# Kernel optimization log

Hardware: AMD Instinct MI355X
Metric: run time of the kernel (lower is better)

## Reference

```python
import jax, jax.numpy as jnp
import numpy as np

N = 500000   # total nodes in batched graph
B = 8192     # number of graphs
H = 128      # hidden_dim
L = 3        # num_layer -> feature_dim F = H*L = 384
F = H * L
S2S_STEPS = 3
VOCAB = 143


def setup_inputs() -> dict:
    key = jax.random.key(0)
    ks = jax.random.split(key, 12)
    sc = 0.02
    unit_type = jax.random.randint(ks[0], (N,), 0, VOCAB)
    # sorted segment ids covering every graph (contiguous, all B segments non-empty)
    node2graph = (jnp.arange(N) * B) // N
    return {
        'unit_type': unit_type,
        'node2graph': node2graph,
        'embed':    jax.random.normal(ks[1], (VOCAB, H)) * sc,
        'msg_W1':   jax.random.normal(ks[2], (H, 2 * H)) * sc,
        'msg_b1':   jnp.zeros((H,)),
        'msg_W2':   jax.random.normal(ks[3], (H, H)) * sc,
        'msg_b2':   jnp.zeros((H,)),
        'gru_Wih':  jax.random.normal(ks[4], (3 * H, H)) * sc,
        'gru_Whh':  jax.random.normal(ks[5], (3 * H, H)) * sc,
        'gru_bih':  jnp.zeros((3 * H,)),
        'gru_bhh':  jnp.zeros((3 * H,)),
        'lstm_Wih': jax.random.normal(ks[6], (4 * F, 2 * F)) * sc,
        'lstm_Whh': jax.random.normal(ks[7], (4 * F, F)) * sc,
        'lstm_bih': jnp.zeros((4 * F,)),
        'lstm_bhh': jnp.zeros((4 * F,)),
    }


def _gru_step(x, h, Wih, Whh, bih, bhh):
    # single-timestep PyTorch GRU cell; gate order r, z, n
    gi = x @ Wih.T + bih
    gh = h @ Whh.T + bhh
    ir, iz, inn = jnp.split(gi, 3, axis=-1)
    hr, hz, hn = jnp.split(gh, 3, axis=-1)
    r = jax.nn.sigmoid(ir + hr)
    z = jax.nn.sigmoid(iz + hz)
    n = jnp.tanh(inn + r * hn)
    return (1.0 - z) * n + z * h


def _lstm_step(x, h, c, Wih, Whh, bih, bhh):
    # single-timestep PyTorch LSTM cell; gate order i, f, g, o
    g = x @ Wih.T + bih + h @ Whh.T + bhh
    i, f, gc, o = jnp.split(g, 4, axis=-1)
    c = jax.nn.sigmoid(f) * c + jax.nn.sigmoid(i) * jnp.tanh(gc)
    h = jax.nn.sigmoid(o) * jnp.tanh(c)
    return h, c


def reference(unit_type, node2graph, embed, msg_W1, msg_b1, msg_W2, msg_b2,
              gru_Wih, gru_Whh, gru_bih, gru_bhh,
              lstm_Wih, lstm_Whh, lstm_bih, lstm_bhh):
    # --- node update stack ---
    layer_input = embed[unit_type]          # [N, H]
    hx = layer_input                        # GRU hidden state (1 layer)
    hiddens = []
    for _ in range(L):
        x2 = jnp.concatenate([layer_input, layer_input], axis=-1)   # [N, 2H]
        msg = jnp.maximum(x2 @ msg_W1.T + msg_b1, 0.0) @ msg_W2.T + msg_b2
        hx = _gru_step(msg, hx, gru_Wih, gru_Whh, gru_bih, gru_bhh)
        hiddens.append(hx)
        layer_input = hx
    node_feature = jnp.concatenate(hiddens, axis=-1)                # [N, F]

    # --- Set2Set readout ---
    h = jnp.zeros((B, F), dtype=node_feature.dtype)
    c = jnp.zeros((B, F), dtype=node_feature.dtype)
    q_star = jnp.zeros((B, 2 * F), dtype=node_feature.dtype)
    for _ in range(S2S_STEPS):
        h, c = _lstm_step(q_star, h, c, lstm_Wih, lstm_Whh, lstm_bih, lstm_bhh)
        q = h                                                       # [B, F]
        logits = jnp.sum(q[node2graph] * node_feature, axis=-1)     # [N]
        m = jax.ops.segment_max(logits, node2graph, num_segments=B,
                                indices_are_sorted=True)
        e = jnp.exp(logits - m[node2graph])
        z = jax.ops.segment_sum(e, node2graph, num_segments=B,
                                indices_are_sorted=True)
        att = e / z[node2graph]                                     # [N]
        pooled = jax.ops.segment_sum(att[:, None] * node_feature, node2graph,
                                     num_segments=B, indices_are_sorted=True)
        q_star = jnp.concatenate([q, pooled], axis=-1)              # [B, 2F]

    return q_star, node_feature
```

## Files before the change

kernel.cpp:

```cpp
#include <hip/hip_runtime.h>

typedef unsigned short u16;
typedef unsigned int   u32;
typedef u16 bfx8 __attribute__((ext_vector_type(8)));
typedef __bf16 bf16x8 __attribute__((ext_vector_type(8)));
typedef float  f32x4  __attribute__((ext_vector_type(4)));

#define NH  128
#define NF  384
#define K2F 768
#define NG4 1536

__device__ __forceinline__ float bf2f(u16 u){ return __uint_as_float(((u32)u) << 16); }
__device__ __forceinline__ u16 f2bf(float f){
  __bf16 h = (__bf16)f;
  return __builtin_bit_cast(u16, h);
}
__device__ __forceinline__ float fsig(float x){ return 1.0f / (1.0f + __expf(-x)); }
__device__ __forceinline__ float ftanh(float x){ return 1.0f - 2.0f / (__expf(2.0f * x) + 1.0f); }

struct P {
  const int *unit_type, *n2g;
  const void *embed, *w1, *b1, *w2, *b2, *gwih, *gwhh, *gbih, *gbhh, *lwih, *lwhh, *lbih, *lbhh;
  int *flag, *segS, *segE;
  u16 *embedB;
  u16 *W1eb, *W2b, *Wihb, *Whhb;
  float *b1f, *b2f, *bihG, *bhhG;
  u16 *WcatB;
  float *bsum;
  float *h1v, *c1v;
  float *hbuf, *cbuf;
  u16 *xcatB;
  float *gout;
  u16 *nfb;
  int useNfb;
  void *out; long qsz;
  int N, B, embedN;
};

__device__ __forceinline__ float ldin(const void* p, long i, int isbf){
  return isbf ? bf2f(((const u16*)p)[i]) : ((const float*)p)[i];
}

__global__ void k_detect(P p){
  __shared__ int cnt;
  if (threadIdx.x == 0) cnt = 0;
  __syncthreads();
  const u32* w = (const u32*)p.embed;
  const int nw = p.embedN / 2;
  int bad = 0;
  for (int i = threadIdx.x; i < nw; i += blockDim.x){
    u32 v = w[i];
    float fhi = __uint_as_float(v & 0xffff0000u);
    float flo = __uint_as_float(v << 16);
    if (!(fabsf(fhi) < 2.0f)) bad++;
    if (!(fabsf(flo) < 2.0f)) bad++;
  }
  atomicAdd(&cnt, bad);
  __syncthreads();
  if (threadIdx.x == 0) *p.flag = (cnt == 0) ? 1 : 0;
}

__global__ void k_prep(P p){
  long o = (long)blockIdx.x * 256 + threadIdx.x;
  const int isbf = *p.flag;
  if (o < p.embedN){ p.embedB[o] = f2bf(ldin(p.embed, o, isbf)); return; } o -= p.embedN;
  if (o < 16384){ long cc = o >> 7, k = o & 127;
    float v = ldin(p.w1, cc*256 + k, isbf) + ldin(p.w1, cc*256 + 128 + k, isbf);
    p.W1eb[o] = f2bf(v); return; } o -= 16384;
  if (o < 16384){ p.W2b[o]  = f2bf(ldin(p.w2, o, isbf));   return; } o -= 16384;
  if (o < 49152){ p.Wihb[o] = f2bf(ldin(p.gwih, o, isbf)); return; } o -= 49152;
  if (o < 49152){ p.Whhb[o] = f2bf(ldin(p.gwhh, o, isbf)); return; } o -= 49152;
  if (o < (long)NG4*K2F){ long j = o / K2F, k = o - j*K2F;
    float v = ldin(p.lwih, o, isbf);
    if (k < NF) v += ldin(p.lwhh, j*NF + k, isbf);
    p.WcatB[o] = f2bf(v); return; } o -= (long)NG4*K2F;
  if (o < NH){ p.b1f[o] = ldin(p.b1, o, isbf); return; } o -= NH;
  if (o < NH){ p.b2f[o] = ldin(p.b2, o, isbf); return; } o -= NH;
  if (o < NF){ p.bihG[o] = ldin(p.gbih, o, isbf); return; } o -= NF;
  if (o < NF){ p.bhhG[o] = ldin(p.gbhh, o, isbf); return; } o -= NF;
  if (o < NG4){ p.bsum[o] = ldin(p.lbih, o, isbf) + ldin(p.lbhh, o, isbf); return; } o -= NG4;
  if (o < p.B){ p.segS[o] = 0; p.segE[o] = 0; }
}

__global__ void k_segb(P p){
  int i = (int)blockIdx.x * 256 + threadIdx.x;
  if (i >= p.N) return;
  int g = p.n2g[i];
  if (g < 0 || g >= p.B) return;
  if (i == 0        || p.n2g[i-1] != g) p.segS[g] = i;
  if (i == p.N - 1  || p.n2g[i+1] != g) p.segE[g] = i + 1;
}

__device__ __forceinline__ f32x4 MF(bf16x8 a, bf16x8 b, f32x4 c){
  return __builtin_amdgcn_mfma_f32_16x16x32_bf16(a, b, c, 0, 0, 0);
}
__device__ __forceinline__ bf16x8 ldA(const u16* buf, int m0, int k0, int lane){
  const int row = m0 + (lane & 15);
  const int byte = (row*256 + (k0 + (lane>>4)*8)*2) ^ ((row&7)<<4);
  return *(const bf16x8*)((const char*)buf + byte);
}
__device__ __forceinline__ bf16x8 ldB(const u16* __restrict__ W, int n0, int k0, int lane){
  return *(const bf16x8*)(W + (long)(n0 + (lane&15))*NH + k0 + (lane>>4)*8);
}
__device__ __forceinline__ bf16x8 ldBs(const u16* __restrict__ W, long stride,
                                       int n0, int k0, int lane){
  return *(const bf16x8*)(W + (long)(n0 + (lane&15))*stride + k0 + (lane>>4)*8);
}
__device__ __forceinline__ void stLDS(u16* buf, int row, int col, float v){
  const int byte = (row*256 + col*2) ^ ((row&7)<<4);
  *(u16*)((char*)buf + byte) = f2bf(v);
}
__device__ __forceinline__ float ldLDS(const u16* buf, int row, int col){
  const int byte = (row*256 + col*2) ^ ((row&7)<<4);
  return bf2f(*(const u16*)((const char*)buf + byte));
}
__device__ __forceinline__ u16 ldLDSraw(const u16* buf, int row, int col){
  const int byte = (row*256 + col*2) ^ ((row&7)<<4);
  return *(const u16*)((const char*)buf + byte);
}

__global__ __launch_bounds__(256, 3) void k_stageA_mfma(P p){
  __shared__ u16 hA[64*128];
  __shared__ u16 mA[64*128];
  __shared__ u16 gA[64*128];
  const int t = (int)threadIdx.x;
  const int lane = t & 63, w = t >> 6;
  const int node0 = (int)blockIdx.x * 64;
  const int cL = lane & 15;
  const int isbf = *p.flag;

  {
    const int row = t >> 2, seg = t & 3;
    const int node = min(node0 + row, p.N - 1);
    int ut = p.unit_type[node];
    ut = min(max(ut, 0), p.embedN/NH - 1);
    const u16* src = p.embedB + (long)ut*NH + seg*32;
    #pragma unroll
    for (int i = 0; i < 4; ++i){
      const int col = seg*32 + i*8;
      const int byte = (row*256 + col*2) ^ ((row&7)<<4);
      *(bfx8*)((char*)hA + byte) = *(const bfx8*)(src + i*8);
    }
  }
  __syncthreads();

  u16*   out16 = (u16*)p.out;
  float* out32 = (float*)p.out;

  #pragma unroll 1
  for (int l = 0; l < 3; ++l){
    {
      f32x4 acc[2][4];
      #pragma unroll
      for (int nt = 0; nt < 2; ++nt){
        const float b = p.b1f[w*32 + nt*16 + cL];
        #pragma unroll
        for (int m = 0; m < 4; ++m) acc[nt][m] = {b,b,b,b};
      }
      for (int k0 = 0; k0 < 128; k0 += 32){
        bf16x8 bv[2];
        #pragma unroll
        for (int nt = 0; nt < 2; ++nt) bv[nt] = ldB(p.W1eb, w*32 + nt*16, k0, lane);
        bf16x8 a[4];
        #pragma unroll
        for (int m = 0; m < 4; ++m) a[m] = ldA(hA, m*16, k0, lane);
        #pragma unroll
        for (int nt = 0; nt < 2; ++nt)
          #pragma unroll
          for (int m = 0; m < 4; ++m) acc[nt][m] = MF(a[m], bv[nt], acc[nt][m]);
      }
      #pragma unroll
      for (int nt = 0; nt < 2; ++nt)
        #pragma unroll
        for (int m = 0; m < 4; ++m)
          #pragma unroll
          for (int j = 0; j < 4; ++j)
            stLDS(mA, m*16 + (lane>>4)*4 + j, w*32 + nt*16 + cL,
                  fmaxf(acc[nt][m][j], 0.0f));
    }
    __syncthreads();
    {
      f32x4 acc[2][4];
      #pragma unroll
      for (int nt = 0; nt < 2; ++nt){
        const float b = p.b2f[w*32 + nt*16 + cL];
        #pragma unroll
        for (int m = 0; m < 4; ++m) acc[nt][m] = {b,b,b,b};
      }
      for (int k0 = 0; k0 < 128; k0 += 32){
        bf16x8 bv[2];
        #pragma unroll
        for (int nt = 0; nt < 2; ++nt) bv[nt] = ldB(p.W2b, w*32 + nt*16, k0, lane);
        bf16x8 a[4];
        #pragma unroll
        for (int m = 0; m < 4; ++m) a[m] = ldA(mA, m*16, k0, lane);
        #pragma unroll
        for (int nt = 0; nt < 2; ++nt)
          #pragma unroll
          for (int m = 0; m < 4; ++m) acc[nt][m] = MF(a[m], bv[nt], acc[nt][m]);
      }
      __syncthreads();
      #pragma unroll
      for (int nt = 0; nt < 2; ++nt)
        #pragma unroll
        for (int m = 0; m < 4; ++m)
          #pragma unroll
          for (int j = 0; j < 4; ++j)
            stLDS(gA, m*16 + (lane>>4)*4 + j, w*32 + nt*16 + cL, acc[nt][m][j]);
    }
    __syncthreads();
    f32x4 rr[2][4];
    {
      f32x4 acc[4][4];
      #pragma unroll
      for (int tc = 0; tc < 4; ++tc){
        const int col = (tc < 2 ? 0 : 128) + w*32 + (tc&1)*16 + cL;
        const float b = p.bihG[col] + p.bhhG[col];
        #pragma unroll
        for (int m = 0; m < 4; ++m) acc[tc][m] = {b,b,b,b};
      }
      for (int k0 = 0; k0 < 128; k0 += 32){
        bf16x8 bv[4];
        #pragma unroll
        for (int tc = 0; tc < 4; ++tc)
          bv[tc] = ldB(p.Wihb, (tc < 2 ? 0 : 128) + w*32 + (tc&1)*16, k0, lane);
        bf16x8 a[4];
        #pragma unroll
        for (int m = 0; m < 4; ++m) a[m] = ldA(gA, m*16, k0, lane);
        #pragma unroll
        for (int tc = 0; tc < 4; ++tc)
          #pragma unroll
          for (int m = 0; m < 4; ++m) acc[tc][m] = MF(a[m], bv[tc], acc[tc][m]);
      }
      for (int k0 = 0; k0 < 128; k0 += 32){
        bf16x8 bv[4];
        #pragma unroll
        for (int tc = 0; tc < 4; ++tc)
          bv[tc] = ldB(p.Whhb, (tc < 2 ? 0 : 128) + w*32 + (tc&1)*16, k0, lane);
        bf16x8 a[4];
        #pragma unroll
        for (int m = 0; m < 4; ++m) a[m] = ldA(hA, m*16, k0, lane);
        #pragma unroll
        for (int tc = 0; tc < 4; ++tc)
          #pragma unroll
          for (int m = 0; m < 4; ++m) acc[tc][m] = MF(a[m], bv[tc], acc[tc][m]);
      }
      #pragma unroll
      for (int nt = 0; nt < 2; ++nt)
        #pragma unroll
        for (int m = 0; m < 4; ++m)
          #pragma unroll
          for (int j = 0; j < 4; ++j){
            rr[nt][m][j] = fsig(acc[nt][m][j]);
            stLDS(mA, m*16 + (lane>>4)*4 + j, w*32 + nt*16 + cL,
                  fsig(acc[nt+2][m][j]));
          }
    }
    {
      f32x4 inn[2][4], hnn[2][4];
      #pragma unroll
      for (int nt = 0; nt < 2; ++nt){
        const int col = 256 + w*32 + nt*16 + cL;
        const float bi = p.bihG[col], bh = p.bhhG[col];
        #pragma unroll
        for (int m = 0; m < 4; ++m){ inn[nt][m] = {bi,bi,bi,bi}; hnn[nt][m] = {bh,bh,bh,bh}; }
      }
      for (int k0 = 0; k0 < 128; k0 += 32){
        bf16x8 bv[2];
        #pragma unroll
        for (int nt = 0; nt < 2; ++nt) bv[nt] = ldB(p.Wihb, 256 + w*32 + nt*16, k0, lane);
        bf16x8 a[4];
        #pragma unroll
        for (int m = 0; m < 4; ++m) a[m] = ldA(gA, m*16, k0, lane);
        #pragma unroll
        for (int nt = 0; nt < 2; ++nt)
          #pragma unroll
          for (int m = 0; m < 4; ++m) inn[nt][m] = MF(a[m], bv[nt], inn[nt][m]);
      }
      for (int k0 = 0; k0 < 128; k0 += 32){
        bf16x8 bv[2];
        #pragma unroll
        for (int nt = 0; nt < 2; ++nt) bv[nt] = ldB(p.Whhb, 256 + w*32 + nt*16, k0, lane);
        bf16x8 a[4];
        #pragma unroll
        for (int m = 0; m < 4; ++m) a[m] = ldA(hA, m*16, k0, lane);
        #pragma unroll
        for (int nt = 0; nt < 2; ++nt)
          #pragma unroll
          for (int m = 0; m < 4; ++m) hnn[nt][m] = MF(a[m], bv[nt], hnn[nt][m]);
      }
      #pragma unroll
      for (int nt = 0; nt < 2; ++nt)
        #pragma unroll
        for (int m = 0; m < 4; ++m)
          #pragma unroll
          for (int j = 0; j < 4; ++j){
            const int row = m*16 + (lane>>4)*4 + j;
            const int col = w*32 + nt*16 + cL;
            const float nn = ftanh(fmaf(rr[nt][m][j], hnn[nt][m][j], inn[nt][m][j]));
            const float zv = ldLDS(mA, row, col);
            const float hv = ldLDS(hA, row, col);
            inn[nt][m][j] = fmaf(zv, hv - nn, nn);
          }
      __syncthreads();
      #pragma unroll
      for (int nt = 0; nt < 2; ++nt)
        #pragma unroll
        for (int m = 0; m < 4; ++m)
          #pragma unroll
          for (int j = 0; j < 4; ++j)
            stLDS(hA, m*16 + (lane>>4)*4 + j, w*32 + nt*16 + cL, inn[nt][m][j]);
      __syncthreads();
    }
    {
      const int col = t & 127;
      const int rh  = t >> 7;
      #pragma unroll 4
      for (int rb = 0; rb < 64; rb += 2){
        const int row = rb + rh;
        const int node = node0 + row;
        if (node < p.N){
          const u16 hv16 = ldLDSraw(hA, row, col);
          const long fi = (long)node*NF + l*NH + col;
          if (isbf){
            __builtin_nontemporal_store(hv16, &out16[p.qsz + fi]);
          } else {
            __builtin_nontemporal_store(bf2f(hv16), &out32[p.qsz + fi]);
            if (p.useNfb) __builtin_nontemporal_store(hv16, &p.nfb[fi]);
          }
        }
      }
    }
  }
}

__global__ void k_lstm0(P p){
  const int d = (int)threadIdx.x;
  if (d >= NF) return;
  const float i_ = fsig(p.bsum[d]);
  const float gc = ftanh(p.bsum[2*NF + d]);
  const float o_ = fsig(p.bsum[3*NF + d]);
  const float cn = i_ * gc;
  p.c1v[d] = cn;
  p.h1v[d] = o_ * ftanh(cn);
}

__global__ __launch_bounds__(256) void k_attn(P p, const float* __restrict__ qsrc,
                                              int qstride, int finalstep){
  __shared__ alignas(16) char raw[32 * NF * 4];
  __shared__ float qs[NF];
  __shared__ float att[32];
  __shared__ float sM, sZ, sSc;

  u16*   nb = (u16*)raw;
  float* nfl = (float*)raw;
  const int t = (int)threadIdx.x;
  const int g = (int)blockIdx.x;
  const int isbf = *p.flag;
  const int bftile = isbf | p.useNfb;
  const u16* nbase = isbf ? (const u16*)p.out + p.qsz : p.nfb;
  const float* o32 = (const float*)p.out;

  for (int i = t; i < NF; i += 256) qs[i] = qsrc[(long)g*qstride + i];
  if (t == 0){ sM = -1e30f; sZ = 0.0f; sSc = 1.0f; }
  int n0 = p.segS[g], n1 = p.segE[g];
  n0 = max(n0, 0); n1 = min(n1, p.N);
  float acc0 = 0.f, acc1 = 0.f;
  __syncthreads();

  for (int base = n0; base < n1; base += 32){
    const int cnt = min(32, n1 - base);
    {
      const int i = t >> 3, q8 = t & 7;
      if (i < cnt){
        if (bftile){
          const bfx8* src = (const bfx8*)(nbase + (long)(base + i)*NF + q8*48);
          #pragma unroll
          for (int j8 = 0; j8 < 6; ++j8)
            *(bfx8*)&nb[i*NF + q8*48 + j8*8] = __builtin_nontemporal_load(src + j8);
        } else {
          const f32x4* src = (const f32x4*)(o32 + p.qsz + (long)(base + i)*NF + q8*48);
          #pragma unroll
          for (int j4 = 0; j4 < 12; ++j4)
            *(f32x4*)&nfl[i*NF + q8*48 + j4*4] = __builtin_nontemporal_load(src + j4);
        }
      }
    }
    __syncthreads();
    {
      const int w = t >> 6, lane = t & 63;
      for (int ii = w; ii < cnt; ii += 4){
        float dot = 0.f;
        #pragma unroll
        for (int j = 0; j < 6; ++j){
          const int d = lane + 64*j;
          const float v = bftile ? bf2f(nb[ii*NF + d]) : nfl[ii*NF + d];
          dot = fmaf(v, qs[d], dot);
        }
        #pragma unroll
        for (int off = 32; off; off >>= 1) dot += __shfl_xor(dot, off);
        if (lane == 0) att[ii] = dot;
      }
    }
    __syncthreads();
    if (t < 32){
      const float l = (t < cnt) ? att[t] : -1e30f;
      float m = l;
      #pragma unroll
      for (int off = 16; off; off >>= 1) m = fmaxf(m, __shfl_xor(m, off));
      const float mnew = fmaxf(sM, m);
      const float e = (t < cnt) ? __expf(l - mnew) : 0.f;
      float z = e;
      #pragma unroll
      for (int off = 16; off; off >>= 1) z += __shfl_xor(z, off);
      if (t < cnt) att[t] = e;
      if (t == 0){
        const float sc = __expf(sM - mnew);
        sSc = sc; sZ = sZ * sc + z; sM = mnew;
      }
    }
    __syncthreads();
    {
      const float sc = sSc;
      acc0 *= sc; acc1 *= sc;
      for (int ii = 0; ii < cnt; ++ii){
        const float a = att[ii];
        const float v0 = bftile ? bf2f(nb[ii*NF + t]) : nfl[ii*NF + t];
        acc0 = fmaf(a, v0, acc0);
        if (t < 128){
          const float v1 = bftile ? bf2f(nb[ii*NF + 256 + t]) : nfl[ii*NF + 256 + t];
          acc1 = fmaf(a, v1, acc1);
        }
      }
    }
    __syncthreads();
  }

  const float invZ = (sZ != 0.0f) ? 1.0f / sZ : 0.0f;
  const float p0 = acc0 * invZ, p1 = acc1 * invZ;
  if (!finalstep){
    u16* xr = p.xcatB + (long)g * K2F;
    xr[t] = f2bf(qs[t]);
    if (t < 128) xr[256 + t] = f2bf(qs[256 + t]);
    xr[NF + t] = f2bf(p0);
    if (t < 128) xr[NF + 256 + t] = f2bf(p1);
  } else {
    const long rb = (long)g * K2F;
    if (isbf){
      u16* o = (u16*)p.out;
      o[rb + t] = f2bf(qs[t]);
      if (t < 128) o[rb + 256 + t] = f2bf(qs[256 + t]);
      o[rb + NF + t] = f2bf(p0);
      if (t < 128) o[rb + NF + 256 + t] = f2bf(p1);
    } else {
      float* o = (float*)p.out;
      o[rb + t] = qs[t];
      if (t < 128) o[rb + 256 + t] = qs[256 + t];
      o[rb + NF + t] = p0;
      if (t < 128) o[rb + NF + 256 + t] = p1;
    }
  }
}

__global__ __launch_bounds__(256, 4) void k_gemm_mfma(P p){
  __shared__ u16 aT[64*128];
  const int t = (int)threadIdx.x;
  const int lane = t & 63, w = t >> 6, cL = lane & 15;
  const int row0 = (int)blockIdx.x * 64, col0 = (int)blockIdx.y * 128;

  f32x4 acc[2][4];
  #pragma unroll
  for (int nt = 0; nt < 2; ++nt)
    #pragma unroll
    for (int m = 0; m < 4; ++m) acc[nt][m] = {0.f,0.f,0.f,0.f};

  for (int kc = 0; kc < K2F; kc += 128){
    __syncthreads();
    {
      const int row = t >> 2, seg = t & 3;
      const int gr = row0 + row;
      const u16* src = p.xcatB + (long)gr*K2F + kc + seg*32;
      #pragma unroll
      for (int i = 0; i < 4; ++i){
        const int col = seg*32 + i*8;
        const int byte = (row*256 + col*2) ^ ((row&7)<<4);
        bfx8 v = {0,0,0,0,0,0,0,0};
        if (gr < p.B) v = *(const bfx8*)(src + i*8);
        *(bfx8*)((char*)aT + byte) = v;
      }
    }
    __syncthreads();
    for (int k0 = 0; k0 < 128; k0 += 32){
      bf16x8 bv[2];
      #pragma unroll
      for (int nt = 0; nt < 2; ++nt)
        bv[nt] = ldBs(p.WcatB, K2F, col0 + w*32 + nt*16, kc + k0, lane);
      bf16x8 a[4];
      #pragma unroll
      for (int m = 0; m < 4; ++m) a[m] = ldA(aT, m*16, k0, lane);
      #pragma unroll
      for (int nt = 0; nt < 2; ++nt)
        #pragma unroll
        for (int m = 0; m < 4; ++m) acc[nt][m] = MF(a[m], bv[nt], acc[nt][m]);
    }
  }
  #pragma unroll
  for (int nt = 0; nt < 2; ++nt){
    const int col = col0 + w*32 + nt*16 + cL;
    const float bs = p.bsum[col];
    #pragma unroll
    for (int m = 0; m < 4; ++m)
      #pragma unroll
      for (int j = 0; j < 4; ++j){
        const int row = row0 + m*16 + (lane>>4)*4 + j;
        if (row < p.B) p.gout[(long)row*NG4 + col] = acc[nt][m][j] + bs;
      }
  }
}

__global__ void k_gates(P p, const float* __restrict__ csrc, int cstride){
  const long idx = (long)blockIdx.x * 256 + threadIdx.x;
  if (idx >= (long)p.B * NF) return;
  const int g = (int)(idx / NF), d = (int)(idx - (long)g*NF);
  const float* gr = p.gout + (long)g*NG4;
  const float i_ = fsig(gr[d]);
  const float f_ = fsig(gr[NF + d]);
  const float gc = ftanh(gr[2*NF + d]);
  const float o_ = fsig(gr[3*NF + d]);
  const float cp = csrc[(long)g*cstride + d];
  const float cn = fmaf(f_, cp, i_ * gc);
  p.cbuf[(long)g*NF + d] = cn;
  p.hbuf[(long)g*NF + d] = o_ * ftanh(cn);
}

extern "C" void kernel_launch(void* const* d_in, const int* in_sizes, int n_in,
                              void* d_out, int out_size, void* d_ws, size_t ws_size,
                              hipStream_t stream){
  P p{};
  p.unit_type = (const int*)d_in[0];
  p.n2g  = (const int*)d_in[1];
  p.embed = d_in[2];  p.w1 = d_in[3];  p.b1 = d_in[4];  p.w2 = d_in[5];  p.b2 = d_in[6];
  p.gwih = d_in[7];  p.gwhh = d_in[8]; p.gbih = d_in[9]; p.gbhh = d_in[10];
  p.lwih = d_in[11]; p.lwhh = d_in[12]; p.lbih = d_in[13]; p.lbhh = d_in[14];

  const int N = in_sizes[0];
  const int B = (int)(((long)out_size - (long)N*NF) / K2F);
  p.N = N; p.B = B; p.embedN = in_sizes[2];
  p.out = d_out; p.qsz = (long)B * K2F;

  char* w = (char*)d_ws;
  size_t used = 0;
  auto alloc = [&](size_t bytes) -> char* {
    char* r = w + used;
    used += (bytes + 255) & ~(size_t)255;
    return r;
  };
  p.flag  = (int*)alloc(4);
  p.segS  = (int*)alloc((size_t)B*4);
  p.segE  = (int*)alloc((size_t)B*4);
  p.embedB= (u16*)  alloc((size_t)p.embedN*2);
  p.W1eb  = (u16*)  alloc(16384*2);
  p.W2b   = (u16*)  alloc(16384*2);
  p.Wihb  = (u16*)  alloc(49152*2);
  p.Whhb  = (u16*)  alloc(49152*2);
  p.b1f   = (float*)alloc(NH*4);
  p.b2f   = (float*)alloc(NH*4);
  p.bihG  = (float*)alloc(NF*4);
  p.bhhG  = (float*)alloc(NF*4);
  p.WcatB = (u16*)  alloc((size_t)NG4*K2F*2);
  p.bsum  = (float*)alloc(NG4*4);
  p.h1v   = (float*)alloc(NF*4);
  p.c1v   = (float*)alloc(NF*4);
  p.hbuf  = (float*)alloc((size_t)B*NF*4);
  p.cbuf  = (float*)alloc((size_t)B*NF*4);
  p.xcatB = (u16*)  alloc((size_t)B*K2F*2);
  p.gout  = (float*)alloc((size_t)B*NG4*4);
  if (used > ws_size){
    (void)hipMemsetAsync(d_out, 0, (size_t)out_size * 2, stream);
    return;
  }
  const size_t nfbBytes = (size_t)N * NF * 2;
  if (used + nfbBytes + 256 <= ws_size){
    p.nfb = (u16*)alloc(nfbBytes);
    p.useNfb = 1;
  } else {
    p.nfb = (u16*)p.flag;
    p.useNfb = 0;
  }

  const long prepTot = (long)p.embedN + 16384 + 16384 + 49152 + 49152
                     + (long)NG4*K2F + NH + NH + NF + NF + NG4 + B;

  k_detect<<<1, 256, 0, stream>>>(p);
  k_prep  <<<(int)((prepTot + 255)/256), 256, 0, stream>>>(p);
  k_segb  <<<(N + 255)/256, 256, 0, stream>>>(p);
  k_stageA_mfma<<<(N + 63)/64, 256, 0, stream>>>(p);
  k_lstm0 <<<1, NF, 0, stream>>>(p);

  const dim3 gemmG((B + 63)/64, NG4/128);
  k_attn <<<B, 256, 0, stream>>>(p, p.h1v, 0, 0);
  k_gemm_mfma<<<gemmG, 256, 0, stream>>>(p);
  k_gates<<<(int)(((long)B*NF + 255)/256), 256, 0, stream>>>(p, p.c1v, 0);
  k_attn <<<B, 256, 0, stream>>>(p, p.hbuf, NF, 0);
  k_gemm_mfma<<<gemmG, 256, 0, stream>>>(p);
  k_gates<<<(int)(((long)B*NF + 255)/256), 256, 0, stream>>>(p, p.cbuf, NF);
  k_attn <<<B, 256, 0, stream>>>(p, p.hbuf, NF, 1);
}
```

Measured before the change: 1.948 ms.

## Fuse LSTM gate nonlinearity into GEMM epilogue and merge segment-bounds into prep

The LSTM gate GEMM is remapped so each block computes the i, f, g and o columns for the same 32 hidden units, one gate per wave. Results are exchanged through shared memory and the cell/hidden update is done in the epilogue. This removes the large fp32 gate buffer round-trip and the separate gates kernel launch, at the cost of extra LDS use and lower occupancy (launch bounds 3). Segment boundary detection is folded into the prep kernel, which drops one launch but also drops the zero-initialisation of segment starts and ends, so every segment must be non-empty.

```diff
diff --git a/kernel.cpp b/kernel.cpp
--- a/kernel.cpp
+++ b/kernel.cpp
@@ -31,7 +31,6 @@
   float *h1v, *c1v;
   float *hbuf, *cbuf;
   u16 *xcatB;
-  float *gout;
   u16 *nfb;
   int useNfb;
   void *out; long qsz;
@@ -80,16 +79,14 @@
   if (o < NF){ p.bihG[o] = ldin(p.gbih, o, isbf); return; } o -= NF;
   if (o < NF){ p.bhhG[o] = ldin(p.gbhh, o, isbf); return; } o -= NF;
   if (o < NG4){ p.bsum[o] = ldin(p.lbih, o, isbf) + ldin(p.lbhh, o, isbf); return; } o -= NG4;
-  if (o < p.B){ p.segS[o] = 0; p.segE[o] = 0; }
-}
-
-__global__ void k_segb(P p){
-  int i = (int)blockIdx.x * 256 + threadIdx.x;
-  if (i >= p.N) return;
-  int g = p.n2g[i];
-  if (g < 0 || g >= p.B) return;
-  if (i == 0        || p.n2g[i-1] != g) p.segS[g] = i;
-  if (i == p.N - 1  || p.n2g[i+1] != g) p.segE[g] = i + 1;
+  if (o < p.N){
+    const int i = (int)o;
+    const int g = p.n2g[i];
+    if (g >= 0 && g < p.B){
+      if (i == 0        || p.n2g[i-1] != g) p.segS[g] = i;
+      if (i == p.N - 1  || p.n2g[i+1] != g) p.segE[g] = i + 1;
+    }
+  }
 }
 
 __device__ __forceinline__ f32x4 MF(bf16x8 a, bf16x8 b, f32x4 c){
@@ -463,11 +460,14 @@
   }
 }
 
-__global__ __launch_bounds__(256, 4) void k_gemm_mfma(P p){
+__global__ __launch_bounds__(256, 3) void k_gemm_fused(P p, const float* __restrict__ csrc,
+                                                       int cstride){
   __shared__ u16 aT[64*128];
+  __shared__ float xch[4*64*32];
   const int t = (int)threadIdx.x;
   const int lane = t & 63, w = t >> 6, cL = lane & 15;
-  const int row0 = (int)blockIdx.x * 64, col0 = (int)blockIdx.y * 128;
+  const int row0 = (int)blockIdx.x * 64;
+  const int d0 = (int)blockIdx.y * 32;
 
   f32x4 acc[2][4];
   #pragma unroll
@@ -495,7 +495,7 @@
       bf16x8 bv[2];
       #pragma unroll
       for (int nt = 0; nt < 2; ++nt)
-        bv[nt] = ldBs(p.WcatB, K2F, col0 + w*32 + nt*16, kc + k0, lane);
+        bv[nt] = ldBs(p.WcatB, K2F, w*NF + d0 + nt*16, kc + k0, lane);
       bf16x8 a[4];
       #pragma unroll
       for (int m = 0; m < 4; ++m) a[m] = ldA(aT, m*16, k0, lane);
@@ -507,31 +507,37 @@
   }
   #pragma unroll
   for (int nt = 0; nt < 2; ++nt){
-    const int col = col0 + w*32 + nt*16 + cL;
-    const float bs = p.bsum[col];
+    const float bs = p.bsum[w*NF + d0 + nt*16 + cL];
     #pragma unroll
     for (int m = 0; m < 4; ++m)
       #pragma unroll
       for (int j = 0; j < 4; ++j){
-        const int row = row0 + m*16 + (lane>>4)*4 + j;
-        if (row < p.B) p.gout[(long)row*NG4 + col] = acc[nt][m][j] + bs;
-      }
-  }
-}
-
-__global__ void k_gates(P p, const float* __restrict__ csrc, int cstride){
-  const long idx = (long)blockIdx.x * 256 + threadIdx.x;
-  if (idx >= (long)p.B * NF) return;
-  const int g = (int)(idx / NF), d = (int)(idx - (long)g*NF);
-  const float* gr = p.gout + (long)g*NG4;
-  const float i_ = fsig(gr[d]);
-  const float f_ = fsig(gr[NF + d]);
-  const float gc = ftanh(gr[2*NF + d]);
-  const float o_ = fsig(gr[3*NF + d]);
-  const float cp = csrc[(long)g*cstride + d];
-  const float cn = fmaf(f_, cp, i_ * gc);
-  p.cbuf[(long)g*NF + d] = cn;
-  p.hbuf[(long)g*NF + d] = o_ * ftanh(cn);
+        const int row = m*16 + (lane>>4)*4 + j;
+        const int col = nt*16 + cL;
+        xch[(w*64 + row)*32 + col] = acc[nt][m][j] + bs;
+      }
+  }
+  __syncthreads();
+  {
+    const int col = t & 31;
+    const int rb2 = (t >> 5) * 8;
+    const int d = d0 + col;
+    #pragma unroll
+    for (int r = 0; r < 8; ++r){
+      const int row = rb2 + r;
+      const int grow = row0 + row;
+      if (grow < p.B){
+        const float i_ = fsig (xch[(0*64 + row)*32 + col]);
+        const float f_ = fsig (xch[(1*64 + row)*32 + col]);
+        const float g_ = ftanh(xch[(2*64 + row)*32 + col]);
+        const float o_ = fsig (xch[(3*64 + row)*32 + col]);
+        const float cp = csrc[(long)grow*cstride + d];
+        const float cn = fmaf(f_, cp, i_ * g_);
+        p.cbuf[(long)grow*NF + d] = cn;
+        p.hbuf[(long)grow*NF + d] = o_ * ftanh(cn);
+      }
+    }
+  }
 }
 
 extern "C" void kernel_launch(void* const* d_in, const int* in_sizes, int n_in,
@@ -575,7 +581,6 @@
   p.hbuf  = (float*)alloc((size_t)B*NF*4);
   p.cbuf  = (float*)alloc((size_t)B*NF*4);
   p.xcatB = (u16*)  alloc((size_t)B*K2F*2);
-  p.gout  = (float*)alloc((size_t)B*NG4*4);
   if (used > ws_size){
     (void)hipMemsetAsync(d_out, 0, (size_t)out_size * 2, stream);
     return;
@@ -590,20 +595,17 @@
   }
 
   const long prepTot = (long)p.embedN + 16384 + 16384 + 49152 + 49152
-                     + (long)NG4*K2F + NH + NH + NF + NF + NG4 + B;
+                     + (long)NG4*K2F + NH + NH + NF + NF + NG4 + N;
 
   k_detect<<<1, 256, 0, stream>>>(p);
   k_prep  <<<(int)((prepTot + 255)/256), 256, 0, stream>>>(p);
-  k_segb  <<<(N + 255)/256, 256, 0, stream>>>(p);
   k_stageA_mfma<<<(N + 63)/64, 256, 0, stream>>>(p);
   k_lstm0 <<<1, NF, 0, stream>>>(p);
 
-  const dim3 gemmG((B + 63)/64, NG4/128);
+  const dim3 gemmG((B + 63)/64, NF/32);
   k_attn <<<B, 256, 0, stream>>>(p, p.h1v, 0, 0);
-  k_gemm_mfma<<<gemmG, 256, 0, stream>>>(p);
-  k_gates<<<(int)(((long)B*NF + 255)/256), 256, 0, stream>>>(p, p.c1v, 0);
+  k_gemm_fused<<<gemmG, 256, 0, stream>>>(p, p.c1v, 0);
   k_attn <<<B, 256, 0, stream>>>(p, p.hbuf, NF, 0);
-  k_gemm_mfma<<<gemmG, 256, 0, stream>>>(p);
-  k_gates<<<(int)(((long)B*NF + 255)/256), 256, 0, stream>>>(p, p.cbuf, NF);
+  k_gemm_fused<<<gemmG, 256, 0, stream>>>(p, p.cbuf, NF);
   k_attn <<<B, 256, 0, stream>>>(p, p.hbuf, NF, 1);
 }
```

Measured after the change: 1.916 ms. No clear change (-1.6%).
